# Optimization experiments

Measured on AMD Instinct MI355X. Metric: run time of the kernel, lower is better.

Reference implementation:

```python
import jax, jax.numpy as jnp
import numpy as np

SPATIAL_SHAPES = ((80, 80), (40, 40), (20, 20))  # strides 8/16/32 on 640x640
NUM_HEADS = 8
N_POINTS = 4
D_MODEL = 256
OFFSET_SCALE = 0.5
N_LEVELS = len(SPATIAL_SHAPES)
TOTAL_P = N_LEVELS * N_POINTS


def setup_inputs() -> dict:
    key = jax.random.key(0)
    ks = jax.random.split(key, 11)
    B, Q = 32, 300
    S = sum(h * w for h, w in SPATIAL_SHAPES)  # 8400
    d = D_MODEL
    s = 0.02
    return {
        "hidden_states": jax.random.normal(ks[0], (B, Q, d), jnp.float32),
        "encoder_hidden_states": jax.random.normal(ks[1], (B, S, d), jnp.float32),
        "reference_points": jax.random.uniform(ks[2], (B, Q, 1, 4), jnp.float32, 0.1, 0.9),
        "W_off": jax.random.normal(ks[3], (d, NUM_HEADS * TOTAL_P * 2), jnp.float32) * s,
        "b_off": jax.random.normal(ks[4], (NUM_HEADS * TOTAL_P * 2,), jnp.float32) * s,
        "W_attn": jax.random.normal(ks[5], (d, NUM_HEADS * TOTAL_P), jnp.float32) * s,
        "b_attn": jax.random.normal(ks[6], (NUM_HEADS * TOTAL_P,), jnp.float32) * s,
        "W_val": jax.random.normal(ks[7], (d, d), jnp.float32) * s,
        "b_val": jax.random.normal(ks[8], (d,), jnp.float32) * s,
        "W_out": jax.random.normal(ks[9], (d, d), jnp.float32) * s,
        "b_out": jax.random.normal(ks[10], (d,), jnp.float32) * s,
    }


def _bilinear_sample(img, grid):
    # img: (N, H, W, C); grid: (N, Q, P, 2), normalized coords in [-1, 1]
    # torch grid_sample(mode='bilinear', padding_mode='zeros', align_corners=False)
    N, Hh, Ww, C = img.shape
    gx = (grid[..., 0] + 1.0) * (Ww * 0.5) - 0.5
    gy = (grid[..., 1] + 1.0) * (Hh * 0.5) - 0.5
    x0 = jnp.floor(gx)
    y0 = jnp.floor(gy)
    wx1 = gx - x0
    wx0 = 1.0 - wx1
    wy1 = gy - y0
    wy0 = 1.0 - wy1
    n_idx = jnp.arange(N)[:, None, None]

    def tap(ix, iy, w):
        valid = (ix >= 0) & (ix < Ww) & (iy >= 0) & (iy < Hh)
        ixc = jnp.clip(ix, 0, Ww - 1).astype(jnp.int32)
        iyc = jnp.clip(iy, 0, Hh - 1).astype(jnp.int32)
        v = img[n_idx, iyc, ixc]  # (N, Q, P, C)
        return v * (w * valid.astype(w.dtype))[..., None]

    return (tap(x0, y0, wx0 * wy0) + tap(x0 + 1.0, y0, wx1 * wy0)
            + tap(x0, y0 + 1.0, wx0 * wy1) + tap(x0 + 1.0, y0 + 1.0, wx1 * wy1))


def reference(hidden_states, encoder_hidden_states, reference_points,
              W_off, b_off, W_attn, b_attn, W_val, b_val, W_out, b_out):
    B, Q, d = hidden_states.shape
    S = encoder_hidden_states.shape[1]
    H = NUM_HEADS
    C = d // H

    value = (encoder_hidden_states @ W_val + b_val).reshape(B, S, H, C)
    offs = (hidden_states @ W_off + b_off).reshape(B, Q, H, TOTAL_P, 2)
    attn = jax.nn.softmax((hidden_states @ W_attn + b_attn).reshape(B, Q, H, TOTAL_P), axis=-1)

    # 4-d reference points branch (boxes): loc = ref_xy + off * (1/P) * ref_wh * offset_scale
    n_points_scale = jnp.full((TOTAL_P, 1), 1.0 / N_POINTS, hidden_states.dtype)
    loc = (reference_points[:, :, None, :, :2]
           + offs * n_points_scale * reference_points[:, :, None, :, 2:] * OFFSET_SCALE)
    grids = 2.0 * loc - 1.0  # method='default'
    grids = grids.transpose(0, 2, 1, 3, 4).reshape(B * H, Q, TOTAL_P, 2)

    value_bh = value.transpose(0, 2, 1, 3).reshape(B * H, S, C)

    samples = []
    start = 0
    p0 = 0
    for (h, w) in SPATIAL_SHAPES:
        v_l = value_bh[:, start:start + h * w].reshape(B * H, h, w, C)
        g_l = grids[:, :, p0:p0 + N_POINTS]
        samples.append(_bilinear_sample(v_l, g_l))
        start += h * w
        p0 += N_POINTS
    sampled = jnp.concatenate(samples, axis=2)  # (B*H, Q, TOTAL_P, C)

    attn_bh = attn.transpose(0, 2, 1, 3).reshape(B * H, Q, TOTAL_P)
    out = jnp.einsum("nqpc,nqp->nqc", sampled, attn_bh)  # (B*H, Q, C)
    out = out.reshape(B, H, Q, C).transpose(0, 2, 1, 3).reshape(B, Q, H * C)
    return out @ W_out + b_out
```

## Files before the change

kernel.cpp:

```cpp
#include <hip/hip_runtime.h>
#include <hip/hip_fp16.h>

#define DEVI __device__ __forceinline__

typedef _Float16 f16x8 __attribute__((ext_vector_type(8)));
typedef float f32x4 __attribute__((ext_vector_type(4)));

static DEVI unsigned short f2h_u(float f) {
    _Float16 h = (_Float16)f;
    return __builtin_bit_cast(unsigned short, h);
}
static DEVI float h2f_u(unsigned short u) {
    return (float)__builtin_bit_cast(_Float16, u);
}
static DEVI unsigned pk2(float a, float b) {
    return (unsigned)f2h_u(a) | ((unsigned)f2h_u(b) << 16);
}


__global__ __launch_bounds__(256) void prep_weights(
    const float* __restrict__ W_val, const float* __restrict__ W_off,
    const float* __restrict__ W_attn, const float* __restrict__ W_out,
    const float* __restrict__ b_off, const float* __restrict__ b_attn,
    unsigned short* __restrict__ Wvt, unsigned short* __restrict__ Wct,
    unsigned short* __restrict__ Wot, float* __restrict__ cbias)
{
    int idx = blockIdx.x * 256 + threadIdx.x;
    if (idx < 65536) {
        int n = idx >> 8, k = idx & 255;
        Wvt[idx] = f2h_u(W_val[k * 256 + n]);
    } else if (idx < 65536 + 73728) {
        int j = idx - 65536;
        int n = j >> 8, k = j & 255;
        Wct[j] = f2h_u(n < 192 ? W_off[k * 192 + n] : W_attn[k * 96 + (n - 192)]);
    } else if (idx < 204800) {
        int j = idx - 139264;
        int n = j >> 8, k = j & 255;
        Wot[j] = f2h_u(W_out[k * 256 + n]);
    } else if (idx < 205088) {
        int j = idx - 204800;
        cbias[j] = (j < 192) ? b_off[j] : b_attn[j - 192];
    }
}

template<int BN, bool OUT_F16>
__global__ __launch_bounds__(256) void gemm_f16(
    const float* __restrict__ A, const unsigned short* __restrict__ Wt,
    const float* __restrict__ bias, void* __restrict__ outp, int ldo)
{
    constexpr int NI  = BN / 16;
    constexpr int LDA = 40;
    constexpr int LDB = 40;
    constexpr int LDC = BN + 4;
    constexpr int SM1 = 64 * LDA * 2 + BN * LDB * 2;
    constexpr int SM2 = 64 * LDC * 4;
    constexpr int SMEM = SM1 > SM2 ? SM1 : SM2;
    __shared__ __align__(16) char smem[SMEM];
    unsigned short* As = (unsigned short*)smem;
    unsigned short* Bs = (unsigned short*)(smem + 64 * LDA * 2);
    float* Cs = (float*)smem;

    const int tid  = threadIdx.x;
    const int wave = tid >> 6;
    const int lane = tid & 63;
    const int l15  = lane & 15;
    const int qd   = lane >> 4;
    const int m0   = blockIdx.y * 64;
    const int n0   = blockIdx.x * BN;

    f32x4 acc[NI];
#pragma unroll
    for (int i = 0; i < NI; i++) acc[i] = (f32x4){0.f, 0.f, 0.f, 0.f};

#pragma unroll
    for (int kt = 0; kt < 8; kt++) {
#pragma unroll
        for (int i = 0; i < 2; i++) {
            int f = tid + i * 256;
            int row = f >> 3, c4 = f & 7;
            const float4 v = *(const float4*)(A + (size_t)(m0 + row) * 256 + kt * 32 + c4 * 4);
            uint2 p;
            p.x = pk2(v.x, v.y);
            p.y = pk2(v.z, v.w);
            *(uint2*)&As[row * LDA + c4 * 4] = p;
        }
        for (int f = tid; f < BN * 4; f += 256) {
            int row = f >> 2, ch = f & 3;
            uint4 v = *(const uint4*)(Wt + (size_t)(n0 + row) * 256 + kt * 32 + ch * 8);
            *(uint4*)&Bs[row * LDB + ch * 8] = v;
        }
        __syncthreads();
        f16x8 af = *(const f16x8*)&As[(wave * 16 + l15) * LDA + qd * 8];
#pragma unroll
        for (int ni = 0; ni < NI; ni++) {
            f16x8 fb = *(const f16x8*)&Bs[(ni * 16 + l15) * LDB + qd * 8];
            acc[ni] = __builtin_amdgcn_mfma_f32_16x16x32_f16(af, fb, acc[ni], 0, 0, 0);
        }
        __syncthreads();
    }

#pragma unroll
    for (int ni = 0; ni < NI; ni++) {
#pragma unroll
        for (int r = 0; r < 4; r++) {
            Cs[(wave * 16 + qd * 4 + r) * LDC + ni * 16 + l15] = acc[ni][r];
        }
    }
    __syncthreads();
    for (int f = tid; f < 64 * (BN / 4); f += 256) {
        int row = f / (BN / 4), c4 = f % (BN / 4);
        float4 v = *(const float4*)&Cs[row * LDC + c4 * 4];
        const float4 bb = *(const float4*)(bias + n0 + c4 * 4);
        v.x += bb.x; v.y += bb.y; v.z += bb.z; v.w += bb.w;
        if (OUT_F16) {
            uint2 p;
            p.x = pk2(v.x, v.y);
            p.y = pk2(v.z, v.w);
            *(uint2*)((unsigned short*)outp + (size_t)(m0 + row) * ldo + n0 + c4 * 4) = p;
        } else {
            *(float4*)((float*)outp + (size_t)(m0 + row) * ldo + n0 + c4 * 4) = v;
        }
    }
}

__global__ __launch_bounds__(256) void sample_attn(
    const float* __restrict__ P, const float* __restrict__ refp,
    const unsigned short* __restrict__ val, float* __restrict__ out_attn)
{
    __shared__ float sLog[8][12];
    __shared__ float sLoc[8][12][3];
    const int row = blockIdx.x;
    const int b = row / 300;
    const int tid = threadIdx.x;

    const float4 r4 = *(const float4*)(refp + (size_t)row * 4);

    int h = 0, p = 0;
    float offx = 0.f, offy = 0.f, logit = 0.f;
    if (tid < 96) {
        h = tid / 12;
        p = tid - h * 12;
        const float* Pr = P + (size_t)row * 288;
        offx  = Pr[h * 24 + p * 2];
        offy  = Pr[h * 24 + p * 2 + 1];
        logit = Pr[192 + h * 12 + p];
        sLog[h][p] = logit;
    }
    __syncthreads();
    if (tid < 96) {
        float m = -1e30f;
#pragma unroll
        for (int j = 0; j < 12; j++) m = fmaxf(m, sLog[h][j]);
        float s = 0.f;
#pragma unroll
        for (int j = 0; j < 12; j++) s += expf(sLog[h][j] - m);
        float w = expf(logit - m) / s;
        sLoc[h][p][0] = r4.x + offx * 0.125f * r4.z;
        sLoc[h][p][1] = r4.y + offy * 0.125f * r4.w;
        sLoc[h][p][2] = w;
    }
    __syncthreads();

    const int hh = tid >> 5, c = tid & 31;
    const unsigned short* vb = val + (size_t)b * 8400 * 256 + hh * 32 + c;
    float acc = 0.f;
#pragma unroll
    for (int p2 = 0; p2 < 12; p2++) {
        const int lvl  = p2 >> 2;
        const int W    = (lvl == 0) ? 80 : ((lvl == 1) ? 40 : 20);
        const int Hh   = W;
        const int loff = (lvl == 0) ? 0 : ((lvl == 1) ? 6400 : 8000);
        const float lx = sLoc[hh][p2][0];
        const float ly = sLoc[hh][p2][1];
        const float w  = sLoc[hh][p2][2];
        const float px = lx * (float)W - 0.5f;
        const float py = ly * (float)Hh - 0.5f;
        const float x0f = floorf(px), y0f = floorf(py);
        const float fx = px - x0f, fy = py - y0f;
        const int x0 = (int)x0f, y0 = (int)y0f;
        const int x1 = x0 + 1, y1 = y0 + 1;
        const float w00 = (1.f - fx) * (1.f - fy);
        const float w10 = fx * (1.f - fy);
        const float w01 = (1.f - fx) * fy;
        const float w11 = fx * fy;
        const bool vx0 = (x0 >= 0) && (x0 < W);
        const bool vx1 = (x1 >= 0) && (x1 < W);
        const bool vy0 = (y0 >= 0) && (y0 < Hh);
        const bool vy1 = (y1 >= 0) && (y1 < Hh);
        const int x0c = min(max(x0, 0), W - 1), x1c = min(max(x1, 0), W - 1);
        const int y0c = min(max(y0, 0), Hh - 1), y1c = min(max(y1, 0), Hh - 1);
        const float v00 = h2f_u(vb[(size_t)(loff + y0c * W + x0c) * 256]);
        const float v10 = h2f_u(vb[(size_t)(loff + y0c * W + x1c) * 256]);
        const float v01 = h2f_u(vb[(size_t)(loff + y1c * W + x0c) * 256]);
        const float v11 = h2f_u(vb[(size_t)(loff + y1c * W + x1c) * 256]);
        float sv = 0.f;
        sv += (vx0 && vy0) ? w00 * v00 : 0.f;
        sv += (vx1 && vy0) ? w10 * v10 : 0.f;
        sv += (vx0 && vy1) ? w01 * v01 : 0.f;
        sv += (vx1 && vy1) ? w11 * v11 : 0.f;
        acc += w * sv;
    }
    out_attn[(size_t)row * 256 + tid] = acc;
}

extern "C" void kernel_launch(void* const* d_in, const int* in_sizes, int n_in,
                              void* d_out, int out_size, void* d_ws, size_t ws_size,
                              hipStream_t stream)
{
    const float* hs     = (const float*)d_in[0];
    const float* enc    = (const float*)d_in[1];
    const float* refp   = (const float*)d_in[2];
    const float* W_off  = (const float*)d_in[3];
    const float* b_off  = (const float*)d_in[4];
    const float* W_attn = (const float*)d_in[5];
    const float* b_attn = (const float*)d_in[6];
    const float* W_val  = (const float*)d_in[7];
    const float* b_val  = (const float*)d_in[8];
    const float* W_out  = (const float*)d_in[9];
    const float* b_out  = (const float*)d_in[10];
    float* outp = (float*)d_out;

    char* ws = (char*)d_ws;
    unsigned short* val = (unsigned short*)ws;
    float* P            = (float*)(ws + 137625600);
    float* oattn        = (float*)(ws + 148684800);
    unsigned short* Wvt = (unsigned short*)(ws + 158515200);
    unsigned short* Wct = (unsigned short*)(ws + 158646272);
    unsigned short* Wot = (unsigned short*)(ws + 158793728);
    float* cbias        = (float*)(ws + 158924800);

    prep_weights<<<802, 256, 0, stream>>>(W_val, W_off, W_attn, W_out,
                                          b_off, b_attn, Wvt, Wct, Wot, cbias);
    gemm_f16<144, false><<<dim3(2, 150), 256, 0, stream>>>(hs, Wct, cbias, P, 288);
    gemm_f16<128, true ><<<dim3(2, 4200), 256, 0, stream>>>(enc, Wvt, b_val, val, 256);
    sample_attn<<<9600, 256, 0, stream>>>(P, refp, val, oattn);
    gemm_f16<128, false><<<dim3(2, 150), 256, 0, stream>>>(oattn, Wot, b_out, outp, 256);
}
```

Before: 543.0 us.

## Add dedicated value-projection GEMM with LDS-direct weight loads and vectorise sampling

Adds a dedicated value-projection kernel. Each block reads its A rows once into registers as f16 and computes all 256 output columns. Weights are pre-swizzled and loaded straight into LDS with global_load_lds, so the activation matrix is no longer re-read and converted once per N tile. The sampling kernel now handles two query rows per block and two channels per thread with 32-bit gathers, and it computes the softmax directly from global memory. The small GEMMs use narrower N tiles so more blocks are launched, at the cost of more redundant A reads.

Result: faster. 477.4 us (-12.1%).

```diff
diff --git a/kernel.cpp b/kernel.cpp
--- a/kernel.cpp
+++ b/kernel.cpp
@@ -22,13 +22,14 @@
     const float* __restrict__ W_val, const float* __restrict__ W_off,
     const float* __restrict__ W_attn, const float* __restrict__ W_out,
     const float* __restrict__ b_off, const float* __restrict__ b_attn,
-    unsigned short* __restrict__ Wvt, unsigned short* __restrict__ Wct,
+    unsigned short* __restrict__ Wst, unsigned short* __restrict__ Wct,
     unsigned short* __restrict__ Wot, float* __restrict__ cbias)
 {
     int idx = blockIdx.x * 256 + threadIdx.x;
     if (idx < 65536) {
         int n = idx >> 8, k = idx & 255;
-        Wvt[idx] = f2h_u(W_val[k * 256 + n]);
+        Wst[(((n >> 7) * 32 + (k >> 3)) * 128 + (n & 127)) * 8 + (k & 7)] =
+            f2h_u(W_val[k * 256 + n]);
     } else if (idx < 65536 + 73728) {
         int j = idx - 65536;
         int n = j >> 8, k = j & 255;
@@ -43,10 +44,110 @@
     }
 }
 
-template<int BN, bool OUT_F16>
+__global__ __launch_bounds__(256, 2) void gemm_value(
+    const float* __restrict__ A, const unsigned short* __restrict__ Wst,
+    const float* __restrict__ bias, unsigned short* __restrict__ out)
+{
+    __shared__ __align__(16) unsigned short Bs[32 * 128 * 8];
+    const int tid  = threadIdx.x;
+    const int wave = tid >> 6;
+    const int lane = tid & 63;
+    const int l15  = lane & 15;
+    const int qd   = lane >> 4;
+    const size_t m0 = (size_t)blockIdx.x * 64;
+
+#pragma unroll
+    for (int it = 0; it < 16; ++it) {
+        const int c = wave * 16 + it;
+        const unsigned short* gp = Wst + c * 512 + lane * 8;
+        unsigned short* lp = Bs + c * 512;
+        __builtin_amdgcn_global_load_lds(
+            (const __attribute__((address_space(1))) void*)gp,
+            (__attribute__((address_space(3))) void*)lp, 16, 0, 0);
+    }
+
+    const float* arow = A + (m0 + wave * 16 + l15) * 256 + qd * 8;
+    float4 a0[8], a1[8];
+#pragma unroll
+    for (int kt = 0; kt < 8; ++kt) {
+        a0[kt] = *(const float4*)(arow + kt * 32);
+        a1[kt] = *(const float4*)(arow + kt * 32 + 4);
+    }
+    f16x8 af[8];
+#pragma unroll
+    for (int kt = 0; kt < 8; ++kt) {
+        union { f16x8 v; uint4 u; } t;
+        t.u.x = pk2(a0[kt].x, a0[kt].y);
+        t.u.y = pk2(a0[kt].z, a0[kt].w);
+        t.u.z = pk2(a1[kt].x, a1[kt].y);
+        t.u.w = pk2(a1[kt].z, a1[kt].w);
+        af[kt] = t.v;
+    }
+
+    f32x4 acc[2][8];
+#pragma unroll
+    for (int h = 0; h < 2; ++h)
+#pragma unroll
+        for (int i = 0; i < 8; ++i) acc[h][i] = (f32x4){0.f, 0.f, 0.f, 0.f};
+
+    __syncthreads();
+
+#pragma unroll
+    for (int kt = 0; kt < 8; ++kt) {
+#pragma unroll
+        for (int ni = 0; ni < 8; ++ni) {
+            f16x8 bf = *(const f16x8*)&Bs[(((kt * 4 + qd) * 128) + ni * 16 + l15) * 8];
+            acc[0][ni] = __builtin_amdgcn_mfma_f32_16x16x32_f16(af[kt], bf, acc[0][ni], 0, 0, 0);
+        }
+    }
+    __syncthreads();
+
+#pragma unroll
+    for (int it = 0; it < 16; ++it) {
+        const int c = wave * 16 + it;
+        const unsigned short* gp = Wst + 32768 + c * 512 + lane * 8;
+        unsigned short* lp = Bs + c * 512;
+        __builtin_amdgcn_global_load_lds(
+            (const __attribute__((address_space(1))) void*)gp,
+            (__attribute__((address_space(3))) void*)lp, 16, 0, 0);
+    }
+    __syncthreads();
+#pragma unroll
+    for (int kt = 0; kt < 8; ++kt) {
+#pragma unroll
+        for (int ni = 0; ni < 8; ++ni) {
+            f16x8 bf = *(const f16x8*)&Bs[(((kt * 4 + qd) * 128) + ni * 16 + l15) * 8];
+            acc[1][ni] = __builtin_amdgcn_mfma_f32_16x16x32_f16(af[kt], bf, acc[1][ni], 0, 0, 0);
+        }
+    }
+
+    constexpr int LDH = 136;
+#pragma unroll
+    for (int h = 0; h < 2; ++h) {
+        __syncthreads();
+        unsigned short* Ch = Bs;
+#pragma unroll
+        for (int ni = 0; ni < 8; ++ni) {
+            const float bb = bias[h * 128 + ni * 16 + l15];
+#pragma unroll
+            for (int r = 0; r < 4; ++r) {
+                Ch[(wave * 16 + qd * 4 + r) * LDH + ni * 16 + l15] =
+                    f2h_u(acc[h][ni][r] + bb);
+            }
+        }
+        __syncthreads();
+        for (int f = tid; f < 64 * 16; f += 256) {
+            int row = f >> 4, c8 = f & 15;
+            uint4 v = *(uint4*)&Ch[row * LDH + c8 * 8];
+            *(uint4*)(out + (m0 + row) * 256 + h * 128 + c8 * 8) = v;
+        }
+    }
+}
+
+template<int BN>
 __global__ __launch_bounds__(256) void gemm_f16(
     const float* __restrict__ A, const unsigned short* __restrict__ Wt,
-    const float* __restrict__ bias, void* __restrict__ outp, int ldo)
+    const float* __restrict__ bias, float* __restrict__ outp, int ldo)
 {
     constexpr int NI  = BN / 16;
     constexpr int LDA = 40;
@@ -90,11 +191,11 @@
             *(uint4*)&Bs[row * LDB + ch * 8] = v;
         }
         __syncthreads();
-        f16x8 af = *(const f16x8*)&As[(wave * 16 + l15) * LDA + qd * 8];
+        f16x8 afr = *(const f16x8*)&As[(wave * 16 + l15) * LDA + qd * 8];
 #pragma unroll
         for (int ni = 0; ni < NI; ni++) {
             f16x8 fb = *(const f16x8*)&Bs[(ni * 16 + l15) * LDB + qd * 8];
-            acc[ni] = __builtin_amdgcn_mfma_f32_16x16x32_f16(af, fb, acc[ni], 0, 0, 0);
+            acc[ni] = __builtin_amdgcn_mfma_f32_16x16x32_f16(afr, fb, acc[ni], 0, 0, 0);
         }
         __syncthreads();
     }
@@ -112,14 +213,7 @@
         float4 v = *(const float4*)&Cs[row * LDC + c4 * 4];
         const float4 bb = *(const float4*)(bias + n0 + c4 * 4);
         v.x += bb.x; v.y += bb.y; v.z += bb.z; v.w += bb.w;
-        if (OUT_F16) {
-            uint2 p;
-            p.x = pk2(v.x, v.y);
-            p.y = pk2(v.z, v.w);
-            *(uint2*)((unsigned short*)outp + (size_t)(m0 + row) * ldo + n0 + c4 * 4) = p;
-        } else {
-            *(float4*)((float*)outp + (size_t)(m0 + row) * ldo + n0 + c4 * 4) = v;
-        }
+        *(float4*)(outp + (size_t)(m0 + row) * ldo + n0 + c4 * 4) = v;
     }
 }
 
@@ -127,54 +221,47 @@
     const float* __restrict__ P, const float* __restrict__ refp,
     const unsigned short* __restrict__ val, float* __restrict__ out_attn)
 {
-    __shared__ float sLog[8][12];
-    __shared__ float sLoc[8][12][3];
-    const int row = blockIdx.x;
-    const int b = row / 300;
+    __shared__ float sLoc[2][8][12][3];
     const int tid = threadIdx.x;
+    const int rr  = tid >> 7;
+    const int t   = tid & 127;
+    const int row = blockIdx.x * 2 + rr;
+    const int b   = row / 300;
 
     const float4 r4 = *(const float4*)(refp + (size_t)row * 4);
 
-    int h = 0, p = 0;
-    float offx = 0.f, offy = 0.f, logit = 0.f;
-    if (tid < 96) {
-        h = tid / 12;
-        p = tid - h * 12;
+    if (t < 96) {
+        const int h = t / 12, p = t - h * 12;
         const float* Pr = P + (size_t)row * 288;
-        offx  = Pr[h * 24 + p * 2];
-        offy  = Pr[h * 24 + p * 2 + 1];
-        logit = Pr[192 + h * 12 + p];
-        sLog[h][p] = logit;
-    }
-    __syncthreads();
-    if (tid < 96) {
+        const float offx  = Pr[h * 24 + p * 2];
+        const float offy  = Pr[h * 24 + p * 2 + 1];
         float m = -1e30f;
 #pragma unroll
-        for (int j = 0; j < 12; j++) m = fmaxf(m, sLog[h][j]);
+        for (int j = 0; j < 12; j++) m = fmaxf(m, Pr[192 + h * 12 + j]);
         float s = 0.f;
 #pragma unroll
-        for (int j = 0; j < 12; j++) s += expf(sLog[h][j] - m);
-        float w = expf(logit - m) / s;
-        sLoc[h][p][0] = r4.x + offx * 0.125f * r4.z;
-        sLoc[h][p][1] = r4.y + offy * 0.125f * r4.w;
-        sLoc[h][p][2] = w;
-    }
-    __syncthreads();
-
-    const int hh = tid >> 5, c = tid & 31;
-    const unsigned short* vb = val + (size_t)b * 8400 * 256 + hh * 32 + c;
-    float acc = 0.f;
+        for (int j = 0; j < 12; j++) s += expf(Pr[192 + h * 12 + j] - m);
+        const float w = expf(Pr[192 + h * 12 + p] - m) / s;
+        sLoc[rr][h][p][0] = r4.x + offx * 0.125f * r4.z;
+        sLoc[rr][h][p][1] = r4.y + offy * 0.125f * r4.w;
+        sLoc[rr][h][p][2] = w;
+    }
+    __syncthreads();
+
+    const int hh = t >> 4;
+    const int cp = t & 15;
+    const unsigned short* vb = val + (size_t)b * 8400 * 256 + hh * 32 + cp * 2;
+    float acc0 = 0.f, acc1 = 0.f;
 #pragma unroll
     for (int p2 = 0; p2 < 12; p2++) {
         const int lvl  = p2 >> 2;
         const int W    = (lvl == 0) ? 80 : ((lvl == 1) ? 40 : 20);
-        const int Hh   = W;
         const int loff = (lvl == 0) ? 0 : ((lvl == 1) ? 6400 : 8000);
-        const float lx = sLoc[hh][p2][0];
-        const float ly = sLoc[hh][p2][1];
-        const float w  = sLoc[hh][p2][2];
+        const float lx = sLoc[rr][hh][p2][0];
+        const float ly = sLoc[rr][hh][p2][1];
+        const float w  = sLoc[rr][hh][p2][2];
         const float px = lx * (float)W - 0.5f;
-        const float py = ly * (float)Hh - 0.5f;
+        const float py = ly * (float)W - 0.5f;
         const float x0f = floorf(px), y0f = floorf(py);
         const float fx = px - x0f, fy = py - y0f;
         const int x0 = (int)x0f, y0 = (int)y0f;
@@ -185,22 +272,25 @@
         const float w11 = fx * fy;
         const bool vx0 = (x0 >= 0) && (x0 < W);
         const bool vx1 = (x1 >= 0) && (x1 < W);
-        const bool vy0 = (y0 >= 0) && (y0 < Hh);
-        const bool vy1 = (y1 >= 0) && (y1 < Hh);
+        const bool vy0 = (y0 >= 0) && (y0 < W);
+        const bool vy1 = (y1 >= 0) && (y1 < W);
         const int x0c = min(max(x0, 0), W - 1), x1c = min(max(x1, 0), W - 1);
-        const int y0c = min(max(y0, 0), Hh - 1), y1c = min(max(y1, 0), Hh - 1);
-        const float v00 = h2f_u(vb[(size_t)(loff + y0c * W + x0c) * 256]);
-        const float v10 = h2f_u(vb[(size_t)(loff + y0c * W + x1c) * 256]);
-        const float v01 = h2f_u(vb[(size_t)(loff + y1c * W + x0c) * 256]);
-        const float v11 = h2f_u(vb[(size_t)(loff + y1c * W + x1c) * 256]);
-        float sv = 0.f;
-        sv += (vx0 && vy0) ? w00 * v00 : 0.f;
-        sv += (vx1 && vy0) ? w10 * v10 : 0.f;
-        sv += (vx0 && vy1) ? w01 * v01 : 0.f;
-        sv += (vx1 && vy1) ? w11 * v11 : 0.f;
-        acc += w * sv;
-    }
-    out_attn[(size_t)row * 256 + tid] = acc;
+        const int y0c = min(max(y0, 0), W - 1), y1c = min(max(y1, 0), W - 1);
+        const unsigned u00 = *(const unsigned*)(vb + (size_t)(loff + y0c * W + x0c) * 256);
+        const unsigned u10 = *(const unsigned*)(vb + (size_t)(loff + y0c * W + x1c) * 256);
+        const unsigned u01 = *(const unsigned*)(vb + (size_t)(loff + y1c * W + x0c) * 256);
+        const unsigned u11 = *(const unsigned*)(vb + (size_t)(loff + y1c * W + x1c) * 256);
+        const float k00 = (vx0 && vy0) ? w00 : 0.f;
+        const float k10 = (vx1 && vy0) ? w10 : 0.f;
+        const float k01 = (vx0 && vy1) ? w01 : 0.f;
+        const float k11 = (vx1 && vy1) ? w11 : 0.f;
+        acc0 += w * (k00 * h2f_u(u00 & 0xffff) + k10 * h2f_u(u10 & 0xffff)
+                   + k01 * h2f_u(u01 & 0xffff) + k11 * h2f_u(u11 & 0xffff));
+        acc1 += w * (k00 * h2f_u(u00 >> 16) + k10 * h2f_u(u10 >> 16)
+                   + k01 * h2f_u(u01 >> 16) + k11 * h2f_u(u11 >> 16));
+    }
+    float2 o; o.x = acc0; o.y = acc1;
+    *(float2*)(out_attn + (size_t)row * 256 + hh * 32 + cp * 2) = o;
 }
 
 extern "C" void kernel_launch(void* const* d_in, const int* in_sizes, int n_in,
@@ -224,15 +314,15 @@
     unsigned short* val = (unsigned short*)ws;
     float* P            = (float*)(ws + 137625600);
     float* oattn        = (float*)(ws + 148684800);
-    unsigned short* Wvt = (unsigned short*)(ws + 158515200);
+    unsigned short* Wst = (unsigned short*)(ws + 158515200);
     unsigned short* Wct = (unsigned short*)(ws + 158646272);
     unsigned short* Wot = (unsigned short*)(ws + 158793728);
     float* cbias        = (float*)(ws + 158924800);
 
     prep_weights<<<802, 256, 0, stream>>>(W_val, W_off, W_attn, W_out,
-                                          b_off, b_attn, Wvt, Wct, Wot, cbias);
-    gemm_f16<144, false><<<dim3(2, 150), 256, 0, stream>>>(hs, Wct, cbias, P, 288);
-    gemm_f16<128, true ><<<dim3(2, 4200), 256, 0, stream>>>(enc, Wvt, b_val, val, 256);
-    sample_attn<<<9600, 256, 0, stream>>>(P, refp, val, oattn);
-    gemm_f16<128, false><<<dim3(2, 150), 256, 0, stream>>>(oattn, Wot, b_out, outp, 256);
-}
+                                          b_off, b_attn, Wst, Wct, Wot, cbias);
+    gemm_f16<96><<<dim3(3, 150), 256, 0, stream>>>(hs, Wct, cbias, P, 288);
+    gemm_value<<<4200, 256, 0, stream>>>(enc, Wst, b_val, val);
+    sample_attn<<<4800, 256, 0, stream>>>(P, refp, val, oattn);
+    gemm_f16<64><<<dim3(4, 150), 256, 0, stream>>>(oattn, Wot, b_out, outp, 256);
+}
```
